# Kernel tuning notes

Hardware: AMD Instinct MI355X
Metric: run time of the kernel (lower is better)

The kernel has to match this reference:

```python
import jax, jax.numpy as jnp
import numpy as np

K = 100000
M = 512

def setup_inputs() -> dict:
    key = jax.random.key(0)
    k1, k2, k3, k4 = jax.random.split(key, 4)
    x = jax.random.normal(k1, (K, M), dtype=jnp.float32)
    # nn.Linear(m, m): weight [m, m], bias [m]
    W = jax.random.normal(k2, (M, M), dtype=jnp.float32) * (1.0 / np.sqrt(M))
    b = jax.random.normal(k3, (M,), dtype=jnp.float32) * 0.01
    # attention vector a: [2m, 1], xavier-normal-like scale
    a = jax.random.normal(k4, (2 * M, 1), dtype=jnp.float32) * np.sqrt(2.0 / (2 * M + 1))
    return {"x": x, "W": W, "b": b, "a": a}

def reference(x, W, b, a):
    # h = Linear(x): [k, m]
    h = x @ W.T + b
    h_mean = jnp.mean(h, axis=0)            # [m]
    a1 = a[:M, 0]                           # [m], applied to h[i]
    a2 = a[M:, 0]                           # [m], applied to h_mean
    # e[i] = a^T cat(h[i], h_mean) -> vectorized as two dot products
    e = h @ a1 + jnp.dot(h_mean, a2)        # [k]
    e = jax.nn.relu(e)
    alpha = jax.nn.softmax(e, axis=0)       # [k]
    # weighted sum of ORIGINAL features (feat = x, pre-linear)
    return jnp.sum(x * alpha[:, None], axis=0)  # [m]
```

## Files before the change

kernel.cpp:

```cpp
#include <hip/hip_runtime.h>
#include <math.h>

#define MM 512
#define KK 100000
#define NB1 1024
#define NW  (NB1 * 4)
#define NOUT 16


__device__ inline float waveSum(float v){
  #pragma unroll
  for(int off = 32; off > 0; off >>= 1) v += __shfl_down(v, off, 64);
  return v;
}
__device__ inline float waveMax(float v){
  #pragma unroll
  for(int off = 32; off > 0; off >>= 1) v = fmaxf(v, __shfl_down(v, off, 64));
  return v;
}
__device__ inline float dot8(float4 x0, float4 x1, float4 v0, float4 v1){
  return x0.x*v0.x + x0.y*v0.y + x0.z*v0.z + x0.w*v0.w
       + x1.x*v1.x + x1.y*v1.y + x1.z*v1.z + x1.w*v1.w;
}

__global__ __launch_bounds__(512) void k_vu(const float* __restrict__ W,
                                            const float* __restrict__ a,
                                            float* __restrict__ v,
                                            float* __restrict__ u){
  int j  = threadIdx.x;
  int k0 = blockIdx.x * 8;
  float pv = 0.f, pu = 0.f;
  #pragma unroll
  for(int kk = 0; kk < 8; kk++){
    float w = W[(size_t)(k0 + kk) * MM + j];
    pv += w * a[k0 + kk];
    pu += w * a[MM + k0 + kk];
  }
  atomicAdd(&v[j], pv);
  atomicAdd(&u[j], pu);
}

__global__ __launch_bounds__(256) void k_pass1(const float* __restrict__ x,
                                               const float* __restrict__ vv,
                                               const float* __restrict__ uu,
                                               float* __restrict__ s,
                                               float* __restrict__ sumU,
                                               float* __restrict__ pmax){
  __shared__ float lsum[4];
  __shared__ float lmax[4];
  int tid  = threadIdx.x;
  int lane = tid & 63;
  int wid  = tid >> 6;
  int gw   = blockIdx.x * 4 + wid;

  const float4* v4 = (const float4*)vv;
  const float4* u4 = (const float4*)uu;
  float4 v0 = v4[lane],      v1 = v4[64 + lane];
  float4 u0 = u4[lane],      u1 = u4[64 + lane];
  float accU = 0.f;
  float wmax = -3.4e38f;

  int myN = (KK - 1 - gw) / NW + 1;
  int k = 0;
  for(; k + 8 <= myN; k += 8){
    float d[8];
    #pragma unroll
    for(int r = 0; r < 8; r++){
      size_t row = (size_t)gw + (size_t)(k + r) * NW;
      const float4* xr = (const float4*)(x + row * MM);
      float4 x0 = xr[lane];
      float4 x1 = xr[64 + lane];
      d[r]  = dot8(x0, x1, v0, v1);
      accU += dot8(x0, x1, u0, u1);
    }
    #pragma unroll
    for(int off = 1; off < 64; off <<= 1){
      #pragma unroll
      for(int r = 0; r < 8; r++) d[r] += __shfl_xor(d[r], off, 64);
    }
    float m01 = fmaxf(fmaxf(d[0], d[1]), fmaxf(d[2], d[3]));
    float m23 = fmaxf(fmaxf(d[4], d[5]), fmaxf(d[6], d[7]));
    wmax = fmaxf(wmax, fmaxf(m01, m23));
    float s0 = (lane & 1) ? d[1] : d[0];
    float s1 = (lane & 1) ? d[3] : d[2];
    float s2 = (lane & 1) ? d[5] : d[4];
    float s3 = (lane & 1) ? d[7] : d[6];
    float t0 = (lane & 2) ? s1 : s0;
    float t1 = (lane & 2) ? s3 : s2;
    float rr = (lane & 4) ? t1 : t0;
    if(lane < 8) s[(size_t)gw + (size_t)(k + lane) * NW] = rr;
  }
  for(; k < myN; k++){
    size_t row = (size_t)gw + (size_t)k * NW;
    const float4* xr = (const float4*)(x + row * MM);
    float4 x0 = xr[lane];
    float4 x1 = xr[64 + lane];
    float d = dot8(x0, x1, v0, v1);
    accU += dot8(x0, x1, u0, u1);
    #pragma unroll
    for(int off = 1; off < 64; off <<= 1) d += __shfl_xor(d, off, 64);
    wmax = fmaxf(wmax, d);
    if(lane == 0) s[row] = d;
  }

  float ws_ = waveSum(accU);
  if(lane == 0){ lsum[wid] = ws_; lmax[wid] = wmax; }
  __syncthreads();
  if(tid == 0){
    atomicAdd(sumU, lsum[0] + lsum[1] + lsum[2] + lsum[3]);
    pmax[blockIdx.x] = fmaxf(fmaxf(lmax[0], lmax[1]), fmaxf(lmax[2], lmax[3]));
  }
}

__global__ __launch_bounds__(256) void k_pass2(const float* __restrict__ x,
                                               const float* __restrict__ s,
                                               const float* __restrict__ b,
                                               const float* __restrict__ a,
                                               const float* __restrict__ sumU,
                                               const float* __restrict__ pmax,
                                               float* __restrict__ part,
                                               float* __restrict__ Z){
  __shared__ float red[8];
  __shared__ float lw[2048];
  int tid  = threadIdx.x;
  int lane = tid & 63;
  int wid  = tid >> 6;
  int gw   = blockIdx.x * 4 + wid;

  float tp = b[tid]       * (a[tid]       + a[MM + tid])
           + b[tid + 256] * (a[tid + 256] + a[MM + tid + 256]);
  float mx = fmaxf(fmaxf(pmax[tid], pmax[tid + 256]),
                   fmaxf(pmax[tid + 512], pmax[tid + 768]));
  float wsum = waveSum(tp);
  mx = waveMax(mx);
  if(lane == 0){ red[wid] = wsum; red[4 + wid] = mx; }
  __syncthreads();
  float c = sumU[0] * (1.0f / (float)KK) + red[0] + red[1] + red[2] + red[3];
  float m = fmaxf(fmaxf(red[4], red[5]), fmaxf(red[6], red[7]));
  m = fmaxf(0.f, m + c);

  float4 a0 = make_float4(0,0,0,0), a1 = make_float4(0,0,0,0);
  float accZ = 0.f;
  int myN = (KK - 1 - gw) / NW + 1;
  int k = 0;
  for(; k + 8 <= myN; k += 8){
    float w[8];
    #pragma unroll
    for(int r = 0; r < 8; r++)
      w[r] = s[(size_t)gw + (size_t)(k + r) * NW];
    #pragma unroll
    for(int r = 0; r < 8; r++){
      w[r] = __expf(fmaxf(w[r] + c, 0.f) - m);
      accZ += w[r];
    }
    #pragma unroll
    for(int r = 0; r < 8; r++){
      size_t row = (size_t)gw + (size_t)(k + r) * NW;
      const float4* xr = (const float4*)(x + row * MM);
      float4 x0 = xr[lane];
      float4 x1 = xr[64 + lane];
      a0.x += w[r] * x0.x; a0.y += w[r] * x0.y; a0.z += w[r] * x0.z; a0.w += w[r] * x0.w;
      a1.x += w[r] * x1.x; a1.y += w[r] * x1.y; a1.z += w[r] * x1.z; a1.w += w[r] * x1.w;
    }
  }
  for(; k < myN; k++){
    size_t row = (size_t)gw + (size_t)k * NW;
    float w = __expf(fmaxf(s[row] + c, 0.f) - m);
    accZ += w;
    const float4* xr = (const float4*)(x + row * MM);
    float4 x0 = xr[lane];
    float4 x1 = xr[64 + lane];
    a0.x += w * x0.x; a0.y += w * x0.y; a0.z += w * x0.z; a0.w += w * x0.w;
    a1.x += w * x1.x; a1.y += w * x1.y; a1.z += w * x1.z; a1.w += w * x1.w;
  }

  float zw = waveSum(accZ);
  __syncthreads();
  float4* lw4 = (float4*)lw;
  lw4[wid * 128 + lane * 2]     = a0;
  lw4[wid * 128 + lane * 2 + 1] = a1;
  if(lane == 0) red[wid] = zw;
  __syncthreads();
  int l = tid >> 2, q = tid & 3;
  float s0 = lw[0*512 + l*8 + q] + lw[1*512 + l*8 + q]
           + lw[2*512 + l*8 + q] + lw[3*512 + l*8 + q];
  float s1 = lw[0*512 + l*8 + 4 + q] + lw[1*512 + l*8 + 4 + q]
           + lw[2*512 + l*8 + 4 + q] + lw[3*512 + l*8 + 4 + q];
  part[(size_t)blockIdx.x * 512 + tid]       = s0;
  part[(size_t)blockIdx.x * 512 + 256 + tid] = s1;
  if(tid == 0)
    atomicAdd(Z, (red[0] + red[1] + red[2] + red[3]) * (1.0f / 64.0f));
}

__global__ __launch_bounds__(256) void k_out(const float* __restrict__ part,
                                             float* __restrict__ acc,
                                             const float* __restrict__ Z,
                                             int* __restrict__ cnt,
                                             float* __restrict__ out){
  __shared__ int lastf;
  int tid = threadIdx.x;
  const float* p = part + (size_t)blockIdx.x * (NB1 / NOUT) * 512;
  float s0 = 0.f, s1 = 0.f;
  #pragma unroll 8
  for(int bb = 0; bb < NB1 / NOUT; bb++){
    s0 += p[bb * 512 + tid];
    s1 += p[bb * 512 + 256 + tid];
  }
  atomicAdd(&acc[tid],       s0);
  atomicAdd(&acc[tid + 256], s1);
  __threadfence();
  if(tid == 0) lastf = (atomicAdd(cnt, 1) == NOUT - 1) ? 1 : 0;
  __syncthreads();
  if(lastf){
    float z = Z[0];
    float v0 = atomicAdd(&acc[tid],       0.0f);
    float v1 = atomicAdd(&acc[tid + 256], 0.0f);
    out[tid]       = v0 / z;
    out[tid + 256] = v1 / z;
  }
}

extern "C" void kernel_launch(void* const* d_in, const int* in_sizes, int n_in,
                              void* d_out, int out_size, void* d_ws, size_t ws_size,
                              hipStream_t stream) {
  const float* x = (const float*)d_in[0];
  const float* W = (const float*)d_in[1];
  const float* b = (const float*)d_in[2];
  const float* a = (const float*)d_in[3];
  float* ws  = (float*)d_ws;
  float* out = (float*)d_out;

  float* v    = ws;
  float* u    = ws + 512;
  float* sumU = ws + 1024;
  float* Z    = ws + 1025;
  int*   cnt  = (int*)(ws + 1026);
  float* acc  = ws + 1536;
  float* pmax = ws + 2048;
  float* s    = ws + 4096;
  float* part = ws + 131072;

  hipMemsetAsync(ws, 0, 2048 * sizeof(float), stream);

  k_vu   <<<64,   512, 0, stream>>>(W, a, v, u);
  k_pass1<<<NB1,  256, 0, stream>>>(x, v, u, s, sumU, pmax);
  k_pass2<<<NB1,  256, 0, stream>>>(x, s, b, a, sumU, pmax, part, Z);
  k_out  <<<NOUT, 256, 0, stream>>>(part, acc, Z, cnt, out);
}
```

Before: 335.8 us.

## Fuse four kernels into one cooperative kernel with grid barriers

Measured after the change: 826.4 us. +146.1%, slower.

```diff
diff --git a/kernel.cpp b/kernel.cpp
--- a/kernel.cpp
+++ b/kernel.cpp
@@ -21,6 +21,212 @@
 __device__ inline float dot8(float4 x0, float4 x1, float4 v0, float4 v1){
   return x0.x*v0.x + x0.y*v0.y + x0.z*v0.z + x0.w*v0.w
        + x1.x*v1.x + x1.y*v1.y + x1.z*v1.z + x1.w*v1.w;
+}
+
+__device__ inline void gridBarrier(int* bar, int tid){
+  __syncthreads();
+  if(tid == 0){
+    __threadfence();
+    atomicAdd(bar, 1);
+    while(__hip_atomic_load(bar, __ATOMIC_ACQUIRE, __HIP_MEMORY_SCOPE_AGENT) < NB1)
+      __builtin_amdgcn_s_sleep(16);
+    __threadfence();
+  }
+  __syncthreads();
+}
+
+__global__ __launch_bounds__(256, 4)
+void k_fused(const float* __restrict__ x, const float* __restrict__ W,
+             const float* __restrict__ bb_, const float* __restrict__ a,
+             float* __restrict__ ws, float* __restrict__ out){
+  float* v    = ws;
+  float* u    = ws + 512;
+  float* sumU = ws + 1024;
+  float* Z    = ws + 1025;
+  int*   cnt  = (int*)(ws + 1026);
+  int*   bar0 = (int*)(ws + 1027);
+  int*   barA = (int*)(ws + 1028);
+  int*   barB = (int*)(ws + 1029);
+  float* acc  = ws + 1536;
+  float* pmax = ws + 2048;
+  float* s    = ws + 4096;
+  float* part = ws + 131072;
+
+  __shared__ float red[8];
+  __shared__ float lw[2048];
+  __shared__ int lastf;
+
+  int tid  = threadIdx.x;
+  int lane = tid & 63;
+  int wid  = tid >> 6;
+  int gw   = blockIdx.x * 4 + wid;
+
+  if(blockIdx.x < 64){
+    int j  = tid;
+    int k0 = blockIdx.x * 8;
+    float pv0 = 0.f, pu0 = 0.f, pv1 = 0.f, pu1 = 0.f;
+    #pragma unroll
+    for(int kk = 0; kk < 8; kk++){
+      float a1v = a[k0 + kk], a2v = a[MM + k0 + kk];
+      float w0 = W[(size_t)(k0 + kk) * MM + j];
+      float w1 = W[(size_t)(k0 + kk) * MM + j + 256];
+      pv0 += w0 * a1v; pu0 += w0 * a2v;
+      pv1 += w1 * a1v; pu1 += w1 * a2v;
+    }
+    atomicAdd(&v[j], pv0);       atomicAdd(&u[j], pu0);
+    atomicAdd(&v[j + 256], pv1); atomicAdd(&u[j + 256], pu1);
+  }
+  gridBarrier(bar0, tid);
+
+  {
+    const float4* v4 = (const float4*)v;
+    const float4* u4 = (const float4*)u;
+    float4 v0 = v4[lane], v1 = v4[64 + lane];
+    float4 u0 = u4[lane], u1 = u4[64 + lane];
+    float accU = 0.f;
+    float wmax = -3.4e38f;
+
+    int myN = (KK - 1 - gw) / NW + 1;
+    int k = 0;
+    for(; k + 8 <= myN; k += 8){
+      float d[8];
+      #pragma unroll
+      for(int r = 0; r < 8; r++){
+        size_t row = (size_t)gw + (size_t)(k + r) * NW;
+        const float4* xr = (const float4*)(x + row * MM);
+        float4 x0 = xr[lane];
+        float4 x1 = xr[64 + lane];
+        d[r]  = dot8(x0, x1, v0, v1);
+        accU += dot8(x0, x1, u0, u1);
+      }
+      #pragma unroll
+      for(int off = 1; off < 64; off <<= 1){
+        #pragma unroll
+        for(int r = 0; r < 8; r++) d[r] += __shfl_xor(d[r], off, 64);
+      }
+      float m01 = fmaxf(fmaxf(d[0], d[1]), fmaxf(d[2], d[3]));
+      float m23 = fmaxf(fmaxf(d[4], d[5]), fmaxf(d[6], d[7]));
+      wmax = fmaxf(wmax, fmaxf(m01, m23));
+      float s0 = (lane & 1) ? d[1] : d[0];
+      float s1 = (lane & 1) ? d[3] : d[2];
+      float s2 = (lane & 1) ? d[5] : d[4];
+      float s3 = (lane & 1) ? d[7] : d[6];
+      float t0 = (lane & 2) ? s1 : s0;
+      float t1 = (lane & 2) ? s3 : s2;
+      float rr = (lane & 4) ? t1 : t0;
+      if(lane < 8) s[(size_t)gw + (size_t)(k + lane) * NW] = rr;
+    }
+    for(; k < myN; k++){
+      size_t row = (size_t)gw + (size_t)k * NW;
+      const float4* xr = (const float4*)(x + row * MM);
+      float4 x0 = xr[lane];
+      float4 x1 = xr[64 + lane];
+      float d = dot8(x0, x1, v0, v1);
+      accU += dot8(x0, x1, u0, u1);
+      #pragma unroll
+      for(int off = 1; off < 64; off <<= 1) d += __shfl_xor(d, off, 64);
+      wmax = fmaxf(wmax, d);
+      if(lane == 0) s[row] = d;
+    }
+
+    float ws_ = waveSum(accU);
+    if(lane == 0){ red[wid] = ws_; red[4 + wid] = wmax; }
+    __syncthreads();
+    if(tid == 0){
+      atomicAdd(sumU, red[0] + red[1] + red[2] + red[3]);
+      pmax[blockIdx.x] = fmaxf(fmaxf(red[4], red[5]), fmaxf(red[6], red[7]));
+    }
+  }
+  gridBarrier(barA, tid);
+
+  {
+    float tp = bb_[tid]       * (a[tid]       + a[MM + tid])
+             + bb_[tid + 256] * (a[tid + 256] + a[MM + tid + 256]);
+    float mx = fmaxf(fmaxf(pmax[tid], pmax[tid + 256]),
+                     fmaxf(pmax[tid + 512], pmax[tid + 768]));
+    float wsum = waveSum(tp);
+    mx = waveMax(mx);
+    if(lane == 0){ red[wid] = wsum; red[4 + wid] = mx; }
+    __syncthreads();
+    float c = sumU[0] * (1.0f / (float)KK) + red[0] + red[1] + red[2] + red[3];
+    float m = fmaxf(fmaxf(red[4], red[5]), fmaxf(red[6], red[7]));
+    m = fmaxf(0.f, m + c);
+
+    float4 a0 = make_float4(0,0,0,0), a1 = make_float4(0,0,0,0);
+    float accZ = 0.f;
+    int myN = (KK - 1 - gw) / NW + 1;
+    int k = 0;
+    for(; k + 8 <= myN; k += 8){
+      float w[8];
+      #pragma unroll
+      for(int r = 0; r < 8; r++)
+        w[r] = s[(size_t)gw + (size_t)(k + r) * NW];
+      #pragma unroll
+      for(int r = 0; r < 8; r++){
+        w[r] = __expf(fmaxf(w[r] + c, 0.f) - m);
+        accZ += w[r];
+      }
+      #pragma unroll
+      for(int r = 0; r < 8; r++){
+        size_t row = (size_t)gw + (size_t)(k + r) * NW;
+        const float4* xr = (const float4*)(x + row * MM);
+        float4 x0 = xr[lane];
+        float4 x1 = xr[64 + lane];
+        a0.x += w[r] * x0.x; a0.y += w[r] * x0.y; a0.z += w[r] * x0.z; a0.w += w[r] * x0.w;
+        a1.x += w[r] * x1.x; a1.y += w[r] * x1.y; a1.z += w[r] * x1.z; a1.w += w[r] * x1.w;
+      }
+    }
+    for(; k < myN; k++){
+      size_t row = (size_t)gw + (size_t)k * NW;
+      float w = __expf(fmaxf(s[row] + c, 0.f) - m);
+      accZ += w;
+      const float4* xr = (const float4*)(x + row * MM);
+      float4 x0 = xr[lane];
+      float4 x1 = xr[64 + lane];
+      a0.x += w * x0.x; a0.y += w * x0.y; a0.z += w * x0.z; a0.w += w * x0.w;
+      a1.x += w * x1.x; a1.y += w * x1.y; a1.z += w * x1.z; a1.w += w * x1.w;
+    }
+
+    float zw = waveSum(accZ);
+    __syncthreads();
+    float4* lw4 = (float4*)lw;
+    lw4[wid * 128 + lane * 2]     = a0;
+    lw4[wid * 128 + lane * 2 + 1] = a1;
+    if(lane == 0) red[wid] = zw;
+    __syncthreads();
+    int l = tid >> 2, q = tid & 3;
+    float s0 = lw[0*512 + l*8 + q] + lw[1*512 + l*8 + q]
+             + lw[2*512 + l*8 + q] + lw[3*512 + l*8 + q];
+    float s1 = lw[0*512 + l*8 + 4 + q] + lw[1*512 + l*8 + 4 + q]
+             + lw[2*512 + l*8 + 4 + q] + lw[3*512 + l*8 + 4 + q];
+    part[(size_t)blockIdx.x * 512 + tid]       = s0;
+    part[(size_t)blockIdx.x * 512 + 256 + tid] = s1;
+    if(tid == 0)
+      atomicAdd(Z, (red[0] + red[1] + red[2] + red[3]) * (1.0f / 64.0f));
+  }
+  gridBarrier(barB, tid);
+
+  if(blockIdx.x < NOUT){
+    const float* p = part + (size_t)blockIdx.x * (NB1 / NOUT) * 512;
+    float s0 = 0.f, s1 = 0.f;
+    #pragma unroll 8
+    for(int bb = 0; bb < NB1 / NOUT; bb++){
+      s0 += p[bb * 512 + tid];
+      s1 += p[bb * 512 + 256 + tid];
+    }
+    atomicAdd(&acc[tid],       s0);
+    atomicAdd(&acc[tid + 256], s1);
+    __threadfence();
+    if(tid == 0) lastf = (atomicAdd(cnt, 1) == NOUT - 1) ? 1 : 0;
+    __syncthreads();
+    if(lastf){
+      float z  = atomicAdd(Z, 0.0f);
+      float v0r = atomicAdd(&acc[tid],       0.0f);
+      float v1r = atomicAdd(&acc[tid + 256], 0.0f);
+      out[tid]       = v0r / z;
+      out[tid + 256] = v1r / z;
+    }
+  }
 }
 
 __global__ __launch_bounds__(512) void k_vu(const float* __restrict__ W,
@@ -230,20 +436,25 @@
   float* ws  = (float*)d_ws;
   float* out = (float*)d_out;
 
-  float* v    = ws;
-  float* u    = ws + 512;
-  float* sumU = ws + 1024;
-  float* Z    = ws + 1025;
-  int*   cnt  = (int*)(ws + 1026);
-  float* acc  = ws + 1536;
-  float* pmax = ws + 2048;
-  float* s    = ws + 4096;
-  float* part = ws + 131072;
-
   hipMemsetAsync(ws, 0, 2048 * sizeof(float), stream);
 
-  k_vu   <<<64,   512, 0, stream>>>(W, a, v, u);
-  k_pass1<<<NB1,  256, 0, stream>>>(x, v, u, s, sumU, pmax);
-  k_pass2<<<NB1,  256, 0, stream>>>(x, s, b, a, sumU, pmax, part, Z);
-  k_out  <<<NOUT, 256, 0, stream>>>(part, acc, Z, cnt, out);
-}
+  void* args[] = {(void*)&x, (void*)&W, (void*)&b, (void*)&a, (void*)&ws, (void*)&out};
+  hipError_t err = hipLaunchCooperativeKernel((const void*)k_fused,
+                                              dim3(NB1), dim3(256),
+                                              args, 0, stream);
+  if(err != hipSuccess){
+    float* v    = ws;
+    float* u    = ws + 512;
+    float* sumU = ws + 1024;
+    float* Z    = ws + 1025;
+    int*   cnt  = (int*)(ws + 1026);
+    float* acc  = ws + 1536;
+    float* pmax = ws + 2048;
+    float* s    = ws + 4096;
+    float* part = ws + 131072;
+    k_vu   <<<64,   512, 0, stream>>>(W, a, v, u);
+    k_pass1<<<NB1,  256, 0, stream>>>(x, v, u, s, sumU, pmax);
+    k_pass2<<<NB1,  256, 0, stream>>>(x, s, b, a, sumU, pmax, part, Z);
+    k_out  <<<NOUT, 256, 0, stream>>>(part, acc, Z, cnt, out);
+  }
+}
```
